# Kernel tuning notes

Measured on AMD Instinct MI355X. Metric: run time of the kernel, lower is better.

## Reference

```python
import jax, jax.numpy as jnp
import numpy as np

B = 512          # batch
IN_UNITS = 8     # primary capsule dim
IN_CH = 1152     # number of primary capsules
NUM_UNITS = 10   # output capsules (classes)
UNIT_SIZE = 16   # output capsule dim
BETA = 1.45      # squash beta: 1.45 - 0.22*(ep_iter/total) with ep_iter = n_iter = 0
NUM_ROUTING = 3


def setup_inputs() -> dict:
    key = jax.random.key(0)
    k1, k2 = jax.random.split(key)
    x = jax.random.normal(k1, (B, IN_UNITS, IN_CH), dtype=jnp.float32)
    # W parameter: torch shape (1, in_channels, num_units, unit_size, in_units); drop leading 1
    W = jax.random.normal(k2, (IN_CH, NUM_UNITS, UNIT_SIZE, IN_UNITS), dtype=jnp.float32)
    return {"x": x, "W": W}


def _squash(s):
    # s: (B, num_units, unit_size). Torch squash sums dim=2 of (B,1,nu,us,1),
    # which is the num_units axis (axis=1 here). Faithful to source.
    mag_sq = jnp.sum(s * s, axis=1, keepdims=True)          # (B,1,us)
    mag = jnp.sqrt(mag_sq)
    return mag_sq / (BETA + mag_sq) * (s / mag)


def reference(x, W):
    # u_hat[b,i,j,u] = sum_k W[i,j,u,k] * x[b,k,i]
    u_hat = jnp.einsum('ijuk,bki->biju', W, x)               # (B, IN_CH, NUM_UNITS, UNIT_SIZE)
    b_ij = jnp.zeros((IN_CH, NUM_UNITS), dtype=x.dtype)
    v = None
    for _ in range(NUM_ROUTING):
        c = jax.nn.softmax(b_ij, axis=0)                     # softmax over in_channels (dim=1 in torch)
        s = jnp.einsum('ij,biju->bju', c, u_hat)             # (B, NUM_UNITS, UNIT_SIZE)
        v = _squash(s)
        # b update: agreement <u_hat, v>, averaged over batch
        b_ij = jnp.einsum('biju,bju->ij', u_hat, v) / u_hat.shape[0]
    # rearrange 'b c (g h) w -> b c g (h w)' with g=4, w=1 -> reshape (B, nu, 4, us//4)
    return v.reshape(v.shape[0], NUM_UNITS, 4, UNIT_SIZE // 4)
```

## Files before the change

kernel.cpp:

```cpp
#include <hip/hip_runtime.h>
#include <hip/hip_bf16.h>
#include <math.h>

#define B    512
#define INU  8
#define IC   1152
#define NU   10
#define US   16
#define JU   160
#define KI   9216
#define BETAC 1.45f
#define NSPLIT 48
#define KC 192
#define NBS 4
#define NP  32

typedef __attribute__((ext_vector_type(8))) __bf16 bf16x8;
typedef __attribute__((ext_vector_type(4))) float floatx4;

static __device__ __forceinline__ unsigned short f2bf(float f) {
  unsigned u = __builtin_bit_cast(unsigned, f);
  u = (u + 0x7fffu + ((u >> 16) & 1u)) >> 16;
  return (unsigned short)u;
}
static __device__ __forceinline__ float bf2f(unsigned short h) {
  return __builtin_bit_cast(float, ((unsigned)h) << 16);
}
static __device__ __forceinline__ uint4 scale8(uint4 wv, float4 cA, float4 cB) {
  union { uint4 u; unsigned short s[8]; } in;
  in.u = wv;
  union { uint4 u; __hip_bfloat162 h[4]; } o;
  o.h[0] = __float22bfloat162_rn(make_float2(bf2f(in.s[0]) * cA.x, bf2f(in.s[1]) * cA.y));
  o.h[1] = __float22bfloat162_rn(make_float2(bf2f(in.s[2]) * cA.z, bf2f(in.s[3]) * cA.w));
  o.h[2] = __float22bfloat162_rn(make_float2(bf2f(in.s[4]) * cB.x, bf2f(in.s[5]) * cB.y));
  o.h[3] = __float22bfloat162_rn(make_float2(bf2f(in.s[6]) * cB.z, bf2f(in.s[7]) * cB.w));
  return o.u;
}

__global__ __launch_bounds__(256) void prep_kernel(
    const float* __restrict__ x, const float* __restrict__ W,
    unsigned short* __restrict__ xb, unsigned short* __restrict__ xT,
    unsigned short* __restrict__ Wt, unsigned short* __restrict__ Wc,
    float* __restrict__ Wr) {
  __shared__ float ts[32 * 322];
  int id = blockIdx.x;
  int t = threadIdx.x;
  if (id < 1152) {
    int k0 = (id % 144) * 64;
    int b0 = (id / 144) * 64;
#pragma unroll
    for (int r = 0; r < 16; ++r) {
      int idx = t + 256 * r;
      int br = idx >> 6, kc = idx & 63;
      float v = x[(size_t)(b0 + br) * KI + k0 + kc];
      ts[br * 65 + kc] = v;
      xb[(size_t)(b0 + br) * KI + k0 + kc] = f2bf(v);
    }
    __syncthreads();
#pragma unroll
    for (int r = 0; r < 8; ++r) {
      int idx = t + 256 * r;
      int kr = idx >> 5, bc = (idx & 31) * 2;
      unsigned lo = f2bf(ts[bc * 65 + kr]);
      unsigned hi = f2bf(ts[(bc + 1) * 65 + kr]);
      *(unsigned*)&xT[(size_t)(k0 + kr) * B + b0 + bc] = lo | (hi << 16);
    }
  } else {
    int wid = id - 1152;
    int i0 = (wid >> 2) * 32;
    int c0 = (wid & 3) * 320;
#pragma unroll
    for (int r = 0; r < 20; ++r) {
      int q = t + 256 * r;
      int il = q / 160, c = (q - il * 160) * 2;
      *(float2*)&ts[il * 322 + c] =
          *(const float2*)&W[(size_t)(i0 + il) * 1280 + c0 + c];
    }
    __syncthreads();
    {
      const float cinv = 1.0f / (float)IC;
      int il2 = (t & 15) * 2;
      for (int p = (t >> 4); p < 320; p += 16) {
        int c = c0 + p;
        int ju = c >> 3, k = c & 7;
        unsigned lo = f2bf(ts[il2 * 322 + p]);
        unsigned hi = f2bf(ts[(il2 + 1) * 322 + p]);
        *(unsigned*)&Wt[(size_t)ju * KI + k * IC + i0 + il2] = lo | (hi << 16);
        unsigned lo2 = f2bf(bf2f((unsigned short)lo) * cinv);
        unsigned hi2 = f2bf(bf2f((unsigned short)hi) * cinv);
        *(unsigned*)&Wc[(size_t)ju * KI + k * IC + i0 + il2] = lo2 | (hi2 << 16);
      }
    }
    int ju0 = c0 >> 3;
    for (int q = t; q < 8 * 32 * 40; q += 256) {
      int k = q / 1280;
      int il = (q / 40) & 31;
      int jl = q - (q / 40) * 40;
      Wr[((size_t)k * IC + i0 + il) * JU + ju0 + jl] = ts[il * 322 + jl * 8 + k];
    }
  }
}

__global__ __launch_bounds__(256) void s_gemm_mfma(
    const unsigned short* __restrict__ xb, const unsigned short* __restrict__ Wc,
    float* __restrict__ sp) {
  int b0 = blockIdx.x * 64;
  int kbase = blockIdx.y * KC;
  int j0 = blockIdx.z * 80;
  int t = threadIdx.x;
  int w = t >> 6, lane = t & 63, col = lane & 15, quad = lane >> 4;
  __shared__ unsigned short xs[2][64 * 40];
  __shared__ unsigned short ms[2][80 * 40];

  int xrow = t >> 2, xc = (t & 3) * 8;
  int mrow0 = t >> 2, mrow1 = 64 + (t >> 2);
  int mc = (t & 3) * 8;

  uint4 xv, m0, m1;
  auto prefetch = [&](int k0) {
    xv = *(const uint4*)&xb[(size_t)(b0 + xrow) * KI + k0 + xc];
    m0 = *(const uint4*)&Wc[(size_t)(j0 + mrow0) * KI + k0 + mc];
    if (t < 64) m1 = *(const uint4*)&Wc[(size_t)(j0 + mrow1) * KI + k0 + mc];
  };
  auto commit = [&](int pb) {
    *(uint4*)&xs[pb][xrow * 40 + xc] = xv;
    *(uint4*)&ms[pb][mrow0 * 40 + mc] = m0;
    if (t < 64) *(uint4*)&ms[pb][mrow1 * 40 + mc] = m1;
  };
  floatx4 acc[5];
#pragma unroll
  for (int jt = 0; jt < 5; ++jt) acc[jt] = (floatx4){0.f, 0.f, 0.f, 0.f};
  const int nsteps = KC >> 5;
  prefetch(kbase);
  commit(0);
  prefetch(kbase + 32);
  for (int s = 0; s < nsteps; ++s) {
    __syncthreads();
    if (s + 1 < nsteps) commit((s + 1) & 1);
    if (s + 2 < nsteps) prefetch(kbase + (s + 2) * 32);
    bf16x8 a = *(bf16x8*)&xs[s & 1][(w * 16 + col) * 40 + quad * 8];
#pragma unroll
    for (int jt = 0; jt < 5; ++jt) {
      bf16x8 bb = *(bf16x8*)&ms[s & 1][(jt * 16 + col) * 40 + quad * 8];
      acc[jt] = __builtin_amdgcn_mfma_f32_16x16x32_bf16(a, bb, acc[jt], 0, 0, 0);
    }
  }
#pragma unroll
  for (int jt = 0; jt < 5; ++jt)
#pragma unroll
    for (int r = 0; r < 4; ++r) {
      int b = b0 + w * 16 + quad * 4 + r;
      sp[((size_t)b * NSPLIT + blockIdx.y) * JU + j0 + jt * 16 + col] = acc[jt][r];
    }
}

__global__ __launch_bounds__(192) void squash_kernel(
    const float* __restrict__ sp, unsigned short* __restrict__ vT,
    float* __restrict__ out) {
  int b = blockIdx.x;
  int t = threadIdx.x;
  __shared__ float sv[JU];
  __shared__ float fac[US];
  float s = 0.0f;
  if (t < JU) {
#pragma unroll
    for (int k = 0; k < NSPLIT; ++k) s += sp[((size_t)b * NSPLIT + k) * JU + t];
    sv[t] = s;
  }
  __syncthreads();
  if (t < US) {
    float m = 0.0f;
#pragma unroll
    for (int j = 0; j < NU; ++j) {
      float q = sv[j * US + t];
      m += q * q;
    }
    fac[t] = sqrtf(m) / (BETAC + m);
  }
  __syncthreads();
  if (t < JU) {
    float val = s * fac[t & 15];
    vT[(size_t)t * B + b] = f2bf(val);
    if (out) out[(size_t)b * JU + t] = val;
  }
}

__global__ __launch_bounds__(256) void b_update_mfma(
    const unsigned short* __restrict__ xT, const unsigned short* __restrict__ vT,
    const float* __restrict__ Wr, float* __restrict__ bp) {
  int k = blockIdx.x / 18;
  int i0 = (blockIdx.x - k * 18) * 64;
  int bs = blockIdx.y;
  int j0 = blockIdx.z * 80;
  size_t ki0 = (size_t)k * IC + i0;
  int t = threadIdx.x;
  int w = t >> 6, lane = t & 63, col = lane & 15, quad = lane >> 4;
  __shared__ unsigned short xs[2][64 * 40];
  __shared__ unsigned short vs[2][80 * 40];
  int xrow = t >> 2, xc = (t & 3) * 8;
  int mrow0 = t >> 2, mrow1 = 64 + (t >> 2);
  int mc = (t & 3) * 8;
  uint4 xv, m0, m1;
  auto prefetch = [&](int c0) {
    xv = *(const uint4*)&xT[(ki0 + xrow) * B + c0 + xc];
    m0 = *(const uint4*)&vT[(size_t)(j0 + mrow0) * B + c0 + mc];
    if (t < 64) m1 = *(const uint4*)&vT[(size_t)(j0 + mrow1) * B + c0 + mc];
  };
  auto commit = [&](int pb) {
    *(uint4*)&xs[pb][xrow * 40 + xc] = xv;
    *(uint4*)&vs[pb][mrow0 * 40 + mc] = m0;
    if (t < 64) *(uint4*)&vs[pb][mrow1 * 40 + mc] = m1;
  };
  floatx4 acc[5];
#pragma unroll
  for (int jt = 0; jt < 5; ++jt) acc[jt] = (floatx4){0.f, 0.f, 0.f, 0.f};
  const int nsteps = (B / NBS) >> 5;
  prefetch(bs * (B / NBS));
  commit(0);
  prefetch(bs * (B / NBS) + 32);
  for (int s = 0; s < nsteps; ++s) {
    __syncthreads();
    if (s + 1 < nsteps) commit((s + 1) & 1);
    if (s + 2 < nsteps) prefetch(bs * (B / NBS) + (s + 2) * 32);
    bf16x8 a = *(bf16x8*)&xs[s & 1][(w * 16 + col) * 40 + quad * 8];
#pragma unroll
    for (int jt = 0; jt < 5; ++jt) {
      bf16x8 bb = *(bf16x8*)&vs[s & 1][(jt * 16 + col) * 40 + quad * 8];
      acc[jt] = __builtin_amdgcn_mfma_f32_16x16x32_bf16(a, bb, acc[jt], 0, 0, 0);
    }
  }
  int p = k * NBS + bs;
  int jb = blockIdx.z * 5;
#pragma unroll
  for (int jt = 0; jt < 5; ++jt) {
#pragma unroll
    for (int r = 0; r < 4; ++r) {
      int i = i0 + w * 16 + quad * 4 + r;
      float wv = Wr[((size_t)k * IC + i) * JU + j0 + jt * 16 + col];
      float pr = wv * acc[jt][r];
      pr += __shfl_xor(pr, 1);
      pr += __shfl_xor(pr, 2);
      pr += __shfl_xor(pr, 4);
      pr += __shfl_xor(pr, 8);
      if (col == 0)
        bp[(size_t)p * (IC * NU) + (jb + jt) * IC + i] = pr * (1.0f / (float)B);
    }
  }
}

__global__ __launch_bounds__(256) void softmax_scale_kernel(
    const float* __restrict__ bp, const unsigned short* __restrict__ Wt,
    unsigned short* __restrict__ Wc) {
  int ju = blockIdx.x;
  int j = ju >> 4;
  int t = threadIdx.x;
  __shared__ float c[IC];
  __shared__ float red[256];
  for (int i = t; i < IC; i += 256) {
    float s = 0.0f;
#pragma unroll
    for (int p = 0; p < NP; ++p) s += bp[(size_t)p * (IC * NU) + j * IC + i];
    c[i] = s;
  }
  __syncthreads();
  float m = -1e30f;
  for (int i = t; i < IC; i += 256) m = fmaxf(m, c[i]);
  red[t] = m;
  __syncthreads();
  for (int o = 128; o > 0; o >>= 1) {
    if (t < o) red[t] = fmaxf(red[t], red[t + o]);
    __syncthreads();
  }
  float mx = red[0];
  __syncthreads();
  float sm = 0.0f;
  for (int i = t; i < IC; i += 256) {
    float e = __expf(c[i] - mx);
    c[i] = e;
    sm += e;
  }
  red[t] = sm;
  __syncthreads();
  for (int o = 128; o > 0; o >>= 1) {
    if (t < o) red[t] += red[t + o];
    __syncthreads();
  }
  float inv = 1.0f / red[0];
  for (int q = t; q < KI / 8; q += 256) {
    int ki = q * 8;
    int i = ki % IC;
    uint4 wv = *(const uint4*)&Wt[(size_t)ju * KI + ki];
    float4 cA = make_float4(c[i] * inv, c[i + 1] * inv, c[i + 2] * inv, c[i + 3] * inv);
    float4 cB = make_float4(c[i + 4] * inv, c[i + 5] * inv, c[i + 6] * inv, c[i + 7] * inv);
    *(uint4*)&Wc[(size_t)ju * KI + ki] = scale8(wv, cA, cB);
  }
}

extern "C" void kernel_launch(void* const* d_in, const int* in_sizes, int n_in,
                              void* d_out, int out_size, void* d_ws,
                              size_t ws_size, hipStream_t stream) {
  const float* x = (const float*)d_in[0];
  const float* W = (const float*)d_in[1];
  float* out = (float*)d_out;

  char* pws = (char*)d_ws;
  float* bp = (float*)pws;                     pws += (size_t)NP * IC * NU * 4;
  float* sp = (float*)pws;                     pws += (size_t)NSPLIT * B * JU * 4;
  float* Wr = (float*)pws;                     pws += (size_t)KI * JU * 4;
  unsigned short* xb = (unsigned short*)pws;   pws += (size_t)B * KI * 2;
  unsigned short* xT = (unsigned short*)pws;   pws += (size_t)KI * B * 2;
  unsigned short* Wt = (unsigned short*)pws;   pws += (size_t)JU * KI * 2;
  unsigned short* Wc = (unsigned short*)pws;   pws += (size_t)JU * KI * 2;
  unsigned short* vT = (unsigned short*)pws;

  prep_kernel<<<1152 + 144, 256, 0, stream>>>(x, W, xb, xT, Wt, Wc, Wr);

  for (int it = 0; it < 3; ++it) {
    s_gemm_mfma<<<dim3(8, NSPLIT, 2), 256, 0, stream>>>(xb, Wc, sp);
    squash_kernel<<<B, 192, 0, stream>>>(sp, vT, (it == 2) ? out : nullptr);
    if (it < 2) {
      b_update_mfma<<<dim3(144, NBS, 2), 256, 0, stream>>>(xT, vT, Wr, bp);
      softmax_scale_kernel<<<160, 256, 0, stream>>>(bp, Wt, Wc);
    }
  }
}
```

Before: 168.8 us.

## Fuse squash into s-GEMM and softmax into b-update via atomic counters

```diff
diff --git a/kernel.cpp b/kernel.cpp
--- a/kernel.cpp
+++ b/kernel.cpp
@@ -10,10 +10,10 @@
 #define JU   160
 #define KI   9216
 #define BETAC 1.45f
-#define NSPLIT 48
-#define KC 192
-#define NBS 4
-#define NP  32
+#define NSPLIT 32
+#define KC 288
+#define NBS 2
+#define NP  16
 
 typedef __attribute__((ext_vector_type(8))) __bf16 bf16x8;
 typedef __attribute__((ext_vector_type(4))) float floatx4;
@@ -41,10 +41,11 @@
     const float* __restrict__ x, const float* __restrict__ W,
     unsigned short* __restrict__ xb, unsigned short* __restrict__ xT,
     unsigned short* __restrict__ Wt, unsigned short* __restrict__ Wc,
-    float* __restrict__ Wr) {
+    float* __restrict__ Wr, int* __restrict__ cnts) {
   __shared__ float ts[32 * 322];
   int id = blockIdx.x;
   int t = threadIdx.x;
+  if (id == 0 && t < 26) cnts[t] = 0;
   if (id < 1152) {
     int k0 = (id % 144) * 64;
     int b0 = (id / 144) * 64;
@@ -101,9 +102,10 @@
   }
 }
 
-__global__ __launch_bounds__(256) void s_gemm_mfma(
+__global__ __launch_bounds__(256) void gs_kernel(
     const unsigned short* __restrict__ xb, const unsigned short* __restrict__ Wc,
-    float* __restrict__ sp) {
+    float* __restrict__ sp, unsigned short* __restrict__ vT,
+    float* __restrict__ out, int* __restrict__ cnt) {
   int b0 = blockIdx.x * 64;
   int kbase = blockIdx.y * KC;
   int j0 = blockIdx.z * 80;
@@ -111,6 +113,8 @@
   int w = t >> 6, lane = t & 63, col = lane & 15, quad = lane >> 4;
   __shared__ unsigned short xs[2][64 * 40];
   __shared__ unsigned short ms[2][80 * 40];
+  __shared__ float sv[2][JU];
+  __shared__ float fac[2][US];
 
   int xrow = t >> 2, xc = (t & 3) * 8;
   int mrow0 = t >> 2, mrow1 = 64 + (t >> 2);
@@ -152,42 +156,59 @@
       int b = b0 + w * 16 + quad * 4 + r;
       sp[((size_t)b * NSPLIT + blockIdx.y) * JU + j0 + jt * 16 + col] = acc[jt][r];
     }
-}
-
-__global__ __launch_bounds__(192) void squash_kernel(
-    const float* __restrict__ sp, unsigned short* __restrict__ vT,
-    float* __restrict__ out) {
-  int b = blockIdx.x;
-  int t = threadIdx.x;
-  __shared__ float sv[JU];
-  __shared__ float fac[US];
-  float s = 0.0f;
+
+  __syncthreads();
+  if (t == 0) {
+    __threadfence();
+    __hip_atomic_fetch_add(cnt + blockIdx.x, 1, __ATOMIC_RELAXED,
+                           __HIP_MEMORY_SCOPE_AGENT);
+  }
+  if (blockIdx.z != 0) return;
+  if (t == 0) {
+    while (__hip_atomic_load(cnt + blockIdx.x, __ATOMIC_RELAXED,
+                             __HIP_MEMORY_SCOPE_AGENT) < 64)
+      __builtin_amdgcn_s_sleep(1);
+    __threadfence();
+  }
+  __syncthreads();
   if (t < JU) {
 #pragma unroll
-    for (int k = 0; k < NSPLIT; ++k) s += sp[((size_t)b * NSPLIT + k) * JU + t];
-    sv[t] = s;
-  }
-  __syncthreads();
-  if (t < US) {
+    for (int bi = 0; bi < 2; ++bi) {
+      int b = b0 + blockIdx.y * 2 + bi;
+      float s = 0.0f;
+#pragma unroll
+      for (int k = 0; k < NSPLIT; ++k) s += sp[((size_t)b * NSPLIT + k) * JU + t];
+      sv[bi][t] = s;
+    }
+  }
+  __syncthreads();
+  if (t < 2 * US) {
+    int bi = t >> 4, u = t & 15;
     float m = 0.0f;
 #pragma unroll
     for (int j = 0; j < NU; ++j) {
-      float q = sv[j * US + t];
+      float q = sv[bi][j * US + u];
       m += q * q;
     }
-    fac[t] = sqrtf(m) / (BETAC + m);
+    fac[bi][u] = sqrtf(m) / (BETAC + m);
   }
   __syncthreads();
   if (t < JU) {
-    float val = s * fac[t & 15];
-    vT[(size_t)t * B + b] = f2bf(val);
-    if (out) out[(size_t)b * JU + t] = val;
-  }
-}
-
-__global__ __launch_bounds__(256) void b_update_mfma(
+#pragma unroll
+    for (int bi = 0; bi < 2; ++bi) {
+      int b = b0 + blockIdx.y * 2 + bi;
+      float val = sv[bi][t] * fac[bi][t & 15];
+      vT[(size_t)t * B + b] = f2bf(val);
+      if (out) out[(size_t)b * JU + t] = val;
+    }
+  }
+}
+
+__global__ __launch_bounds__(256) void uc_kernel(
     const unsigned short* __restrict__ xT, const unsigned short* __restrict__ vT,
-    const float* __restrict__ Wr, float* __restrict__ bp) {
+    const float* __restrict__ Wr, float* __restrict__ bp,
+    const unsigned short* __restrict__ Wt, unsigned short* __restrict__ Wc,
+    int* __restrict__ cnt) {
   int k = blockIdx.x / 18;
   int i0 = (blockIdx.x - k * 18) * 64;
   int bs = blockIdx.y;
@@ -197,6 +218,8 @@
   int w = t >> 6, lane = t & 63, col = lane & 15, quad = lane >> 4;
   __shared__ unsigned short xs[2][64 * 40];
   __shared__ unsigned short vs[2][80 * 40];
+  __shared__ float csm[IC];
+  __shared__ float red[256];
   int xrow = t >> 2, xc = (t & 3) * 8;
   int mrow0 = t >> 2, mrow1 = 64 + (t >> 2);
   int mc = (t & 3) * 8;
@@ -246,25 +269,35 @@
         bp[(size_t)p * (IC * NU) + (jb + jt) * IC + i] = pr * (1.0f / (float)B);
     }
   }
-}
-
-__global__ __launch_bounds__(256) void softmax_scale_kernel(
-    const float* __restrict__ bp, const unsigned short* __restrict__ Wt,
-    unsigned short* __restrict__ Wc) {
-  int ju = blockIdx.x;
-  int j = ju >> 4;
-  int t = threadIdx.x;
-  __shared__ float c[IC];
-  __shared__ float red[256];
+
+  __syncthreads();
+  if (t == 0) {
+    __threadfence();
+    __hip_atomic_fetch_add(cnt, 1, __ATOMIC_RELAXED, __HIP_MEMORY_SCOPE_AGENT);
+  }
+  int ju = -1;
+  if (blockIdx.z == 0) {
+    if (blockIdx.y == 0) ju = blockIdx.x;
+    else if (blockIdx.x < 16) ju = 144 + blockIdx.x;
+  }
+  if (ju < 0) return;
+  if (t == 0) {
+    while (__hip_atomic_load(cnt, __ATOMIC_RELAXED, __HIP_MEMORY_SCOPE_AGENT) <
+           144 * 2 * 2)
+      __builtin_amdgcn_s_sleep(1);
+    __threadfence();
+  }
+  __syncthreads();
+  const int j = ju >> 4;
   for (int i = t; i < IC; i += 256) {
     float s = 0.0f;
 #pragma unroll
-    for (int p = 0; p < NP; ++p) s += bp[(size_t)p * (IC * NU) + j * IC + i];
-    c[i] = s;
+    for (int pp = 0; pp < NP; ++pp) s += bp[(size_t)pp * (IC * NU) + j * IC + i];
+    csm[i] = s;
   }
   __syncthreads();
   float m = -1e30f;
-  for (int i = t; i < IC; i += 256) m = fmaxf(m, c[i]);
+  for (int i = t; i < IC; i += 256) m = fmaxf(m, csm[i]);
   red[t] = m;
   __syncthreads();
   for (int o = 128; o > 0; o >>= 1) {
@@ -275,8 +308,8 @@
   __syncthreads();
   float sm = 0.0f;
   for (int i = t; i < IC; i += 256) {
-    float e = __expf(c[i] - mx);
-    c[i] = e;
+    float e = __expf(csm[i] - mx);
+    csm[i] = e;
     sm += e;
   }
   red[t] = sm;
@@ -290,8 +323,10 @@
     int ki = q * 8;
     int i = ki % IC;
     uint4 wv = *(const uint4*)&Wt[(size_t)ju * KI + ki];
-    float4 cA = make_float4(c[i] * inv, c[i + 1] * inv, c[i + 2] * inv, c[i + 3] * inv);
-    float4 cB = make_float4(c[i + 4] * inv, c[i + 5] * inv, c[i + 6] * inv, c[i + 7] * inv);
+    float4 cA = make_float4(csm[i] * inv, csm[i + 1] * inv,
+                            csm[i + 2] * inv, csm[i + 3] * inv);
+    float4 cB = make_float4(csm[i + 4] * inv, csm[i + 5] * inv,
+                            csm[i + 6] * inv, csm[i + 7] * inv);
     *(uint4*)&Wc[(size_t)ju * KI + ki] = scale8(wv, cA, cB);
   }
 }
@@ -311,16 +346,16 @@
   unsigned short* xT = (unsigned short*)pws;   pws += (size_t)KI * B * 2;
   unsigned short* Wt = (unsigned short*)pws;   pws += (size_t)JU * KI * 2;
   unsigned short* Wc = (unsigned short*)pws;   pws += (size_t)JU * KI * 2;
-  unsigned short* vT = (unsigned short*)pws;
-
-  prep_kernel<<<1152 + 144, 256, 0, stream>>>(x, W, xb, xT, Wt, Wc, Wr);
+  unsigned short* vT = (unsigned short*)pws;   pws += (size_t)JU * B * 2;
+  int* cnts = (int*)pws;
+
+  prep_kernel<<<1152 + 144, 256, 0, stream>>>(x, W, xb, xT, Wt, Wc, Wr, cnts);
 
   for (int it = 0; it < 3; ++it) {
-    s_gemm_mfma<<<dim3(8, NSPLIT, 2), 256, 0, stream>>>(xb, Wc, sp);
-    squash_kernel<<<B, 192, 0, stream>>>(sp, vT, (it == 2) ? out : nullptr);
-    if (it < 2) {
-      b_update_mfma<<<dim3(144, NBS, 2), 256, 0, stream>>>(xT, vT, Wr, bp);
-      softmax_scale_kernel<<<160, 256, 0, stream>>>(bp, Wt, Wc);
-    }
-  }
-}
+    gs_kernel<<<dim3(8, NSPLIT, 2), 256, 0, stream>>>(
+        xb, Wc, sp, vT, (it == 2) ? out : nullptr, cnts + it * 8);
+    if (it < 2)
+      uc_kernel<<<dim3(144, NBS, 2), 256, 0, stream>>>(
+          xT, vT, Wr, bp, Wt, Wc, cnts + 24 + it);
+  }
+}
```

Result: slower. 371.4 us (+120.1%).

## Deepen GEMM prefetch to two stages, vectorize prep, and shrink split counts

Applied to the files above, without the earlier changes.

```diff
diff --git a/kernel.cpp b/kernel.cpp
--- a/kernel.cpp
+++ b/kernel.cpp
@@ -10,10 +10,10 @@
 #define JU   160
 #define KI   9216
 #define BETAC 1.45f
-#define NSPLIT 48
-#define KC 192
-#define NBS 4
-#define NP  32
+#define NSPLIT 32
+#define KC 288
+#define NBS 2
+#define NP  16
 
 typedef __attribute__((ext_vector_type(8))) __bf16 bf16x8;
 typedef __attribute__((ext_vector_type(4))) float floatx4;
@@ -42,27 +42,31 @@
     unsigned short* __restrict__ xb, unsigned short* __restrict__ xT,
     unsigned short* __restrict__ Wt, unsigned short* __restrict__ Wc,
     float* __restrict__ Wr) {
-  __shared__ float ts[32 * 322];
+  __shared__ float ts[32 * 324];
+  unsigned short* tsb = (unsigned short*)ts;
   int id = blockIdx.x;
   int t = threadIdx.x;
   if (id < 1152) {
     int k0 = (id % 144) * 64;
     int b0 = (id / 144) * 64;
 #pragma unroll
-    for (int r = 0; r < 16; ++r) {
+    for (int r = 0; r < 4; ++r) {
       int idx = t + 256 * r;
-      int br = idx >> 6, kc = idx & 63;
-      float v = x[(size_t)(b0 + br) * KI + k0 + kc];
-      ts[br * 65 + kc] = v;
-      xb[(size_t)(b0 + br) * KI + k0 + kc] = f2bf(v);
+      int br = idx >> 4, kc = (idx & 15) * 4;
+      float4 v = *(const float4*)&x[(size_t)(b0 + br) * KI + k0 + kc];
+      ushort4 h;
+      h.x = f2bf(v.x); h.y = f2bf(v.y); h.z = f2bf(v.z); h.w = f2bf(v.w);
+      *(ushort4*)&xb[(size_t)(b0 + br) * KI + k0 + kc] = h;
+      *(unsigned*)&tsb[br * 70 + kc] = (unsigned)h.x | ((unsigned)h.y << 16);
+      *(unsigned*)&tsb[br * 70 + kc + 2] = (unsigned)h.z | ((unsigned)h.w << 16);
     }
     __syncthreads();
 #pragma unroll
     for (int r = 0; r < 8; ++r) {
       int idx = t + 256 * r;
       int kr = idx >> 5, bc = (idx & 31) * 2;
-      unsigned lo = f2bf(ts[bc * 65 + kr]);
-      unsigned hi = f2bf(ts[(bc + 1) * 65 + kr]);
+      unsigned lo = tsb[bc * 70 + kr];
+      unsigned hi = tsb[(bc + 1) * 70 + kr];
       *(unsigned*)&xT[(size_t)(k0 + kr) * B + b0 + bc] = lo | (hi << 16);
     }
   } else {
@@ -70,11 +74,11 @@
     int i0 = (wid >> 2) * 32;
     int c0 = (wid & 3) * 320;
 #pragma unroll
-    for (int r = 0; r < 20; ++r) {
+    for (int r = 0; r < 10; ++r) {
       int q = t + 256 * r;
-      int il = q / 160, c = (q - il * 160) * 2;
-      *(float2*)&ts[il * 322 + c] =
-          *(const float2*)&W[(size_t)(i0 + il) * 1280 + c0 + c];
+      int il = q / 80, c = (q - il * 80) * 4;
+      *(float4*)&ts[il * 324 + c] =
+          *(const float4*)&W[(size_t)(i0 + il) * 1280 + c0 + c];
     }
     __syncthreads();
     {
@@ -83,8 +87,8 @@
       for (int p = (t >> 4); p < 320; p += 16) {
         int c = c0 + p;
         int ju = c >> 3, k = c & 7;
-        unsigned lo = f2bf(ts[il2 * 322 + p]);
-        unsigned hi = f2bf(ts[(il2 + 1) * 322 + p]);
+        unsigned lo = f2bf(ts[il2 * 324 + p]);
+        unsigned hi = f2bf(ts[(il2 + 1) * 324 + p]);
         *(unsigned*)&Wt[(size_t)ju * KI + k * IC + i0 + il2] = lo | (hi << 16);
         unsigned lo2 = f2bf(bf2f((unsigned short)lo) * cinv);
         unsigned hi2 = f2bf(bf2f((unsigned short)hi) * cinv);
@@ -96,7 +100,7 @@
       int k = q / 1280;
       int il = (q / 40) & 31;
       int jl = q - (q / 40) * 40;
-      Wr[((size_t)k * IC + i0 + il) * JU + ju0 + jl] = ts[il * 322 + jl * 8 + k];
+      Wr[((size_t)k * IC + i0 + il) * JU + ju0 + jl] = ts[il * 324 + jl * 8 + k];
     }
   }
 }
@@ -116,28 +120,38 @@
   int mrow0 = t >> 2, mrow1 = 64 + (t >> 2);
   int mc = (t & 3) * 8;
 
-  uint4 xv, m0, m1;
-  auto prefetch = [&](int k0) {
-    xv = *(const uint4*)&xb[(size_t)(b0 + xrow) * KI + k0 + xc];
-    m0 = *(const uint4*)&Wc[(size_t)(j0 + mrow0) * KI + k0 + mc];
-    if (t < 64) m1 = *(const uint4*)&Wc[(size_t)(j0 + mrow1) * KI + k0 + mc];
-  };
-  auto commit = [&](int pb) {
-    *(uint4*)&xs[pb][xrow * 40 + xc] = xv;
-    *(uint4*)&ms[pb][mrow0 * 40 + mc] = m0;
-    if (t < 64) *(uint4*)&ms[pb][mrow1 * 40 + mc] = m1;
-  };
+  uint4 xvA, m0A, m1A, xvB, m0B, m1B, xvC, m0C, m1C;
+#define S_LOAD(X, M0, M1, kk)                                              \
+  do {                                                                     \
+    X = *(const uint4*)&xb[(size_t)(b0 + xrow) * KI + (kk) + xc];          \
+    M0 = *(const uint4*)&Wc[(size_t)(j0 + mrow0) * KI + (kk) + mc];        \
+    if (t < 64) M1 = *(const uint4*)&Wc[(size_t)(j0 + mrow1) * KI + (kk) + mc]; \
+  } while (0)
+#define S_COMMIT(X, M0, M1, pb)                                            \
+  do {                                                                     \
+    *(uint4*)&xs[pb][xrow * 40 + xc] = X;                                  \
+    *(uint4*)&ms[pb][mrow0 * 40 + mc] = M0;                                \
+    if (t < 64) *(uint4*)&ms[pb][mrow1 * 40 + mc] = M1;                    \
+  } while (0)
+
   floatx4 acc[5];
 #pragma unroll
   for (int jt = 0; jt < 5; ++jt) acc[jt] = (floatx4){0.f, 0.f, 0.f, 0.f};
   const int nsteps = KC >> 5;
-  prefetch(kbase);
-  commit(0);
-  prefetch(kbase + 32);
+  S_LOAD(xvA, m0A, m1A, kbase);
+  S_COMMIT(xvA, m0A, m1A, 0);
+  S_LOAD(xvB, m0B, m1B, kbase + 32);
+  S_LOAD(xvC, m0C, m1C, kbase + 64);
+#pragma unroll
   for (int s = 0; s < nsteps; ++s) {
     __syncthreads();
-    if (s + 1 < nsteps) commit((s + 1) & 1);
-    if (s + 2 < nsteps) prefetch(kbase + (s + 2) * 32);
+    if ((s & 1) == 0) {
+      if (s + 1 < nsteps) S_COMMIT(xvB, m0B, m1B, (s + 1) & 1);
+      if (s + 3 < nsteps) S_LOAD(xvB, m0B, m1B, kbase + (s + 3) * 32);
+    } else {
+      if (s + 1 < nsteps) S_COMMIT(xvC, m0C, m1C, (s + 1) & 1);
+      if (s + 3 < nsteps) S_LOAD(xvC, m0C, m1C, kbase + (s + 3) * 32);
+    }
     bf16x8 a = *(bf16x8*)&xs[s & 1][(w * 16 + col) * 40 + quad * 8];
 #pragma unroll
     for (int jt = 0; jt < 5; ++jt) {
@@ -145,6 +159,8 @@
       acc[jt] = __builtin_amdgcn_mfma_f32_16x16x32_bf16(a, bb, acc[jt], 0, 0, 0);
     }
   }
+#undef S_LOAD
+#undef S_COMMIT
 #pragma unroll
   for (int jt = 0; jt < 5; ++jt)
 #pragma unroll
@@ -200,28 +216,40 @@
   int xrow = t >> 2, xc = (t & 3) * 8;
   int mrow0 = t >> 2, mrow1 = 64 + (t >> 2);
   int mc = (t & 3) * 8;
-  uint4 xv, m0, m1;
-  auto prefetch = [&](int c0) {
-    xv = *(const uint4*)&xT[(ki0 + xrow) * B + c0 + xc];
-    m0 = *(const uint4*)&vT[(size_t)(j0 + mrow0) * B + c0 + mc];
-    if (t < 64) m1 = *(const uint4*)&vT[(size_t)(j0 + mrow1) * B + c0 + mc];
-  };
-  auto commit = [&](int pb) {
-    *(uint4*)&xs[pb][xrow * 40 + xc] = xv;
-    *(uint4*)&vs[pb][mrow0 * 40 + mc] = m0;
-    if (t < 64) *(uint4*)&vs[pb][mrow1 * 40 + mc] = m1;
-  };
+  const int cb = bs * (B / NBS);
+
+  uint4 xvA, m0A, m1A, xvB, m0B, m1B, xvC, m0C, m1C;
+#define U_LOAD(X, M0, M1, cc)                                              \
+  do {                                                                     \
+    X = *(const uint4*)&xT[(ki0 + xrow) * B + (cc) + xc];                  \
+    M0 = *(const uint4*)&vT[(size_t)(j0 + mrow0) * B + (cc) + mc];         \
+    if (t < 64) M1 = *(const uint4*)&vT[(size_t)(j0 + mrow1) * B + (cc) + mc]; \
+  } while (0)
+#define U_COMMIT(X, M0, M1, pb)                                            \
+  do {                                                                     \
+    *(uint4*)&xs[pb][xrow * 40 + xc] = X;                                  \
+    *(uint4*)&vs[pb][mrow0 * 40 + mc] = M0;                                \
+    if (t < 64) *(uint4*)&vs[pb][mrow1 * 40 + mc] = M1;                    \
+  } while (0)
+
   floatx4 acc[5];
 #pragma unroll
   for (int jt = 0; jt < 5; ++jt) acc[jt] = (floatx4){0.f, 0.f, 0.f, 0.f};
   const int nsteps = (B / NBS) >> 5;
-  prefetch(bs * (B / NBS));
-  commit(0);
-  prefetch(bs * (B / NBS) + 32);
+  U_LOAD(xvA, m0A, m1A, cb);
+  U_COMMIT(xvA, m0A, m1A, 0);
+  U_LOAD(xvB, m0B, m1B, cb + 32);
+  U_LOAD(xvC, m0C, m1C, cb + 64);
+#pragma unroll
   for (int s = 0; s < nsteps; ++s) {
     __syncthreads();
-    if (s + 1 < nsteps) commit((s + 1) & 1);
-    if (s + 2 < nsteps) prefetch(bs * (B / NBS) + (s + 2) * 32);
+    if ((s & 1) == 0) {
+      if (s + 1 < nsteps) U_COMMIT(xvB, m0B, m1B, (s + 1) & 1);
+      if (s + 3 < nsteps) U_LOAD(xvB, m0B, m1B, cb + (s + 3) * 32);
+    } else {
+      if (s + 1 < nsteps) U_COMMIT(xvC, m0C, m1C, (s + 1) & 1);
+      if (s + 3 < nsteps) U_LOAD(xvC, m0C, m1C, cb + (s + 3) * 32);
+    }
     bf16x8 a = *(bf16x8*)&xs[s & 1][(w * 16 + col) * 40 + quad * 8];
 #pragma unroll
     for (int jt = 0; jt < 5; ++jt) {
@@ -229,6 +257,8 @@
       acc[jt] = __builtin_amdgcn_mfma_f32_16x16x32_bf16(a, bb, acc[jt], 0, 0, 0);
     }
   }
+#undef U_LOAD
+#undef U_COMMIT
   int p = k * NBS + bs;
   int jb = blockIdx.z * 5;
 #pragma unroll
```

After: 160.1 us. 1.05x faster.
